# Optimization experiments

Hardware: AMD Instinct MI355X
Metric: run time of the kernel (lower is better)

## Reference

```python
import jax, jax.numpy as jnp
import numpy as np
from jax import lax

STRIDE = 1
PAD = 1  # module pads 1 on each side whenever padding != 0


def setup_inputs() -> dict:
    key = jax.random.key(0)
    kx, kw, kb = jax.random.split(key, 3)
    x = jax.random.normal(kx, (4096, 4096), dtype=jnp.float32)
    weight = jax.random.normal(kw, (15, 15), dtype=jnp.float32)
    bias = jax.random.normal(kb, (1,), dtype=jnp.float32)
    return {"x": x, "weight": weight, "bias": bias}


def reference(x, weight, bias):
    # Single-channel 2D cross-correlation with constant zero padding of 1 and
    # stride STRIDE, plus a scalar bias. lax.conv_general_dilated computes
    # correlation (no kernel flip), matching the torch corr2d loop exactly.
    out = lax.conv_general_dilated(
        x[None, None, :, :],          # NCHW, N=C=1
        weight[None, None, :, :],      # OIHW, O=I=1
        window_strides=(STRIDE, STRIDE),
        padding=[(PAD, PAD), (PAD, PAD)],
        dimension_numbers=("NCHW", "OIHW", "NCHW"),
    )[0, 0]
    return out + bias[0]
```

## Files before the change

### kernel.cpp

```cpp
#include <hip/hip_runtime.h>

#define IN_N   4096
#define OW     4084
#define KS     15
#define TILE   64
#define XROWS  78
#define XS     88
#define NBX    64
#define NBY    64

typedef __attribute__((ext_vector_type(8))) short     v8s;
typedef __attribute__((ext_vector_type(8))) _Float16  v8h;
typedef __attribute__((ext_vector_type(4))) float     v4f;
typedef __attribute__((ext_vector_type(2))) float     v2f;
typedef __attribute__((ext_vector_type(2))) unsigned  v2u;

__global__ void build_B(const float* __restrict__ w, unsigned short* __restrict__ Bg) {
    int ky = blockIdx.x;
    int e  = threadIdx.x;
    int n = e & 15, quad = e >> 4;
    unsigned short vals[8];
    #pragma unroll
    for (int j = 0; j < 8; ++j) {
        int d = quad * 8 + j - 1 - n;
        _Float16 h = (_Float16)0.0f;
        if (d >= 0 && d < KS) h = (_Float16)w[ky * KS + d];
        union { _Float16 hh; unsigned short u; } cv; cv.hh = h;
        vals[j] = cv.u;
    }
    *(v8s*)(&Bg[(ky * 64 + e) * 8]) = *(const v8s*)vals;
}

__device__ __forceinline__ unsigned pk(float a, float b) {
    return __builtin_bit_cast(unsigned, __builtin_amdgcn_cvt_pkrtz(a, b));
}

__global__ __launch_bounds__(256, 6) void conv2d_mfma10(
    const float* __restrict__ x, const unsigned short* __restrict__ Bg,
    const float* __restrict__ bias, float* __restrict__ out)
{
    __shared__ unsigned short xtile[XROWS * XS] __attribute__((aligned(16)));

    const int tid = threadIdx.x;
    const int bx = blockIdx.x, by = blockIdx.y;
    const int X0 = bx * TILE;
    const int Y0 = by * TILE;
    const bool interior = (bx > 0) & (bx < NBX - 1) & (by > 0) & (by < NBY - 1);

    if (tid < 240) {
        const int tcol = tid % 20;
        const int trow = tid / 20;
        const int c0 = 4 * tcol;
        unsigned short* dst = &xtile[trow * XS + c0];
        if (interior) {
            v2f Ld[7][2];
            const float* xr = x + (size_t)(Y0 - 1 + trow) * IN_N + (X0 - 2 + c0);
            #pragma unroll
            for (int i = 0; i < 7; ++i) {
                if (i < 6 || trow < 6) {
                    Ld[i][0] = *(const v2f*)xr;
                    Ld[i][1] = *(const v2f*)(xr + 2);
                }
                xr += 12 * (size_t)IN_N;
            }
            #pragma unroll
            for (int i = 0; i < 7; ++i) {
                if (i < 6 || trow < 6) {
                    v2u p;
                    p.x = pk(Ld[i][0].x, Ld[i][0].y);
                    p.y = pk(Ld[i][1].x, Ld[i][1].y);
                    *(v2u*)dst = p;
                }
                dst += 12 * XS;
            }
        } else {
            const int gc0 = X0 - 2 + c0;
            #pragma unroll
            for (int i = 0; i < 7; ++i) {
                int row = trow + 12 * i;
                if (row < XROWS) {
                    int gr = Y0 - 1 + row;
                    float f0 = 0.f, f1 = 0.f, f2 = 0.f, f3 = 0.f;
                    if ((unsigned)gr < (unsigned)IN_N) {
                        const float* xr = x + (size_t)gr * IN_N;
                        if ((unsigned)(gc0 + 0) < (unsigned)IN_N) f0 = xr[gc0 + 0];
                        if ((unsigned)(gc0 + 1) < (unsigned)IN_N) f1 = xr[gc0 + 1];
                        if ((unsigned)(gc0 + 2) < (unsigned)IN_N) f2 = xr[gc0 + 2];
                        if ((unsigned)(gc0 + 3) < (unsigned)IN_N) f3 = xr[gc0 + 3];
                    }
                    v2u p;
                    p.x = pk(f0, f1);
                    p.y = pk(f2, f3);
                    *(v2u*)(&xtile[row * XS + c0]) = p;
                }
            }
        }
    }
    __syncthreads();

    const int lane = tid & 63;
    const int wv   = tid >> 6;
    const int m    = lane & 15;
    const int quad = lane >> 4;

    v4f acc[4];
    #pragma unroll
    for (int t = 0; t < 4; ++t) acc[t] = (v4f){0.f, 0.f, 0.f, 0.f};

    const v8h* Bgv = (const v8h*)Bg;
    v8h bcur = Bgv[lane];
    const unsigned short* arow = &xtile[(wv * 16 + m) * XS + quad * 8];

    #pragma unroll
    for (int ky = 0; ky < KS; ++ky) {
        v8h bnext = (ky < KS - 1) ? Bgv[(ky + 1) * 64 + lane] : bcur;
        v8h a0 = *(const v8h*)(arow + 0);
        v8h a1 = *(const v8h*)(arow + 16);
        v8h a2 = *(const v8h*)(arow + 32);
        v8h a3 = *(const v8h*)(arow + 48);
        acc[0] = __builtin_amdgcn_mfma_f32_16x16x32_f16(a0, bcur, acc[0], 0, 0, 0);
        acc[1] = __builtin_amdgcn_mfma_f32_16x16x32_f16(a1, bcur, acc[1], 0, 0, 0);
        acc[2] = __builtin_amdgcn_mfma_f32_16x16x32_f16(a2, bcur, acc[2], 0, 0, 0);
        acc[3] = __builtin_amdgcn_mfma_f32_16x16x32_f16(a3, bcur, acc[3], 0, 0, 0);
        arow += XS;
        bcur = bnext;
    }

    const float bv = bias[0];
    const int orow0 = Y0 + wv * 16 + quad * 4;
    const int ocol0 = X0 + m;
    if (interior | ((bx < NBX - 1) & (by < NBY - 1))) {
        float* o0 = &out[(size_t)orow0 * OW + ocol0];
        #pragma unroll
        for (int t = 0; t < 4; ++t) {
            #pragma unroll
            for (int r = 0; r < 4; ++r)
                o0[(size_t)r * OW + t * 16] = acc[t][r] + bv;
        }
    } else {
        #pragma unroll
        for (int t = 0; t < 4; ++t) {
            int oc = ocol0 + t * 16;
            if (oc < OW) {
                #pragma unroll
                for (int r = 0; r < 4; ++r) {
                    int orow = orow0 + r;
                    if (orow < OW)
                        out[(size_t)orow * OW + oc] = acc[t][r] + bv;
                }
            }
        }
    }
}

extern "C" void kernel_launch(void* const* d_in, const int* in_sizes, int n_in,
                              void* d_out, int out_size, void* d_ws, size_t ws_size,
                              hipStream_t stream) {
    const float* x    = (const float*)d_in[0];
    const float* w    = (const float*)d_in[1];
    const float* bias = (const float*)d_in[2];
    float* out        = (float*)d_out;
    unsigned short* Bg = (unsigned short*)d_ws;

    build_B<<<dim3(KS), dim3(64), 0, stream>>>(w, Bg);
    dim3 grid(NBX, NBY);
    conv2d_mfma10<<<grid, dim3(256), 0, stream>>>(x, Bg, bias, out);
}
```

Baseline: 138.7 us.

## Warp-specialize blocks into staging and compute groups with double-buffered tiles

Each 512-thread block now covers four vertically stacked 64x64 output tiles. Two 256-thread groups alternate roles, one staging the next tile into a second LDS buffer while the other runs MFMA on the current one. The goal is to overlap global loads with matrix compute inside a block. The cost is fewer blocks (a quarter of the grid), half of the threads idle during each phase, a block-wide barrier per step, and doubled LDS per block.

```diff
diff --git a/kernel.cpp b/kernel.cpp
--- a/kernel.cpp
+++ b/kernel.cpp
@@ -6,8 +6,10 @@
 #define TILE   64
 #define XROWS  78
 #define XS     88
+#define TPB    4
 #define NBX    64
-#define NBY    64
+#define NBY    16
+#define NRT    64
 
 typedef __attribute__((ext_vector_type(8))) short     v8s;
 typedef __attribute__((ext_vector_type(8))) _Float16  v8h;
@@ -35,71 +37,60 @@
     return __builtin_bit_cast(unsigned, __builtin_amdgcn_cvt_pkrtz(a, b));
 }
 
-__global__ __launch_bounds__(256, 6) void conv2d_mfma10(
-    const float* __restrict__ x, const unsigned short* __restrict__ Bg,
-    const float* __restrict__ bias, float* __restrict__ out)
+__device__ __forceinline__ void stage_tile(
+    const float* __restrict__ x, unsigned short* __restrict__ buf,
+    int gtid, int R0, int X0, bool fast)
 {
-    __shared__ unsigned short xtile[XROWS * XS] __attribute__((aligned(16)));
-
-    const int tid = threadIdx.x;
-    const int bx = blockIdx.x, by = blockIdx.y;
-    const int X0 = bx * TILE;
-    const int Y0 = by * TILE;
-    const bool interior = (bx > 0) & (bx < NBX - 1) & (by > 0) & (by < NBY - 1);
-
-    if (tid < 240) {
-        const int tcol = tid % 20;
-        const int trow = tid / 20;
-        const int c0 = 4 * tcol;
-        unsigned short* dst = &xtile[trow * XS + c0];
-        if (interior) {
-            v2f Ld[7][2];
-            const float* xr = x + (size_t)(Y0 - 1 + trow) * IN_N + (X0 - 2 + c0);
-            #pragma unroll
-            for (int i = 0; i < 7; ++i) {
-                if (i < 6 || trow < 6) {
-                    Ld[i][0] = *(const v2f*)xr;
-                    Ld[i][1] = *(const v2f*)(xr + 2);
+    if (gtid >= 240) return;
+    const int tcol = gtid % 20;
+    const int trow = gtid / 20;
+    const int c0 = 4 * tcol;
+    unsigned short* dst = &buf[trow * XS + c0];
+    if (fast) {
+        const float* xr = x + (size_t)(R0 - 1 + trow) * IN_N + (X0 - 2 + c0);
+        #pragma unroll
+        for (int i = 0; i < 7; ++i) {
+            if (i < 6 || trow < 6) {
+                v2f f01 = *(const v2f*)xr;
+                v2f f23 = *(const v2f*)(xr + 2);
+                v2u p;
+                p.x = pk(f01.x, f01.y);
+                p.y = pk(f23.x, f23.y);
+                *(v2u*)dst = p;
+            }
+            xr  += 12 * (size_t)IN_N;
+            dst += 12 * XS;
+        }
+    } else {
+        const int gc0 = X0 - 2 + c0;
+        #pragma unroll
+        for (int i = 0; i < 7; ++i) {
+            int row = trow + 12 * i;
+            if (row < XROWS) {
+                int gr = R0 - 1 + row;
+                float f0 = 0.f, f1 = 0.f, f2 = 0.f, f3 = 0.f;
+                if ((unsigned)gr < (unsigned)IN_N) {
+                    const float* xr = x + (size_t)gr * IN_N;
+                    if ((unsigned)(gc0 + 0) < (unsigned)IN_N) f0 = xr[gc0 + 0];
+                    if ((unsigned)(gc0 + 1) < (unsigned)IN_N) f1 = xr[gc0 + 1];
+                    if ((unsigned)(gc0 + 2) < (unsigned)IN_N) f2 = xr[gc0 + 2];
+                    if ((unsigned)(gc0 + 3) < (unsigned)IN_N) f3 = xr[gc0 + 3];
                 }
-                xr += 12 * (size_t)IN_N;
-            }
-            #pragma unroll
-            for (int i = 0; i < 7; ++i) {
-                if (i < 6 || trow < 6) {
-                    v2u p;
-                    p.x = pk(Ld[i][0].x, Ld[i][0].y);
-                    p.y = pk(Ld[i][1].x, Ld[i][1].y);
-                    *(v2u*)dst = p;
-                }
-                dst += 12 * XS;
-            }
-        } else {
-            const int gc0 = X0 - 2 + c0;
-            #pragma unroll
-            for (int i = 0; i < 7; ++i) {
-                int row = trow + 12 * i;
-                if (row < XROWS) {
-                    int gr = Y0 - 1 + row;
-                    float f0 = 0.f, f1 = 0.f, f2 = 0.f, f3 = 0.f;
-                    if ((unsigned)gr < (unsigned)IN_N) {
-                        const float* xr = x + (size_t)gr * IN_N;
-                        if ((unsigned)(gc0 + 0) < (unsigned)IN_N) f0 = xr[gc0 + 0];
-                        if ((unsigned)(gc0 + 1) < (unsigned)IN_N) f1 = xr[gc0 + 1];
-                        if ((unsigned)(gc0 + 2) < (unsigned)IN_N) f2 = xr[gc0 + 2];
-                        if ((unsigned)(gc0 + 3) < (unsigned)IN_N) f3 = xr[gc0 + 3];
-                    }
-                    v2u p;
-                    p.x = pk(f0, f1);
-                    p.y = pk(f2, f3);
-                    *(v2u*)(&xtile[row * XS + c0]) = p;
-                }
+                v2u p;
+                p.x = pk(f0, f1);
+                p.y = pk(f2, f3);
+                *(v2u*)(&buf[row * XS + c0]) = p;
             }
         }
     }
-    __syncthreads();
+}
 
-    const int lane = tid & 63;
-    const int wv   = tid >> 6;
+__device__ __forceinline__ void compute_tile(
+    const unsigned short* __restrict__ buf, const v8h* __restrict__ Bgv,
+    float* __restrict__ out, float bv, int gtid, int R0, int X0, bool safe)
+{
+    const int lane = gtid & 63;
+    const int wv   = gtid >> 6;
     const int m    = lane & 15;
     const int quad = lane >> 4;
 
@@ -107,9 +98,8 @@
     #pragma unroll
     for (int t = 0; t < 4; ++t) acc[t] = (v4f){0.f, 0.f, 0.f, 0.f};
 
-    const v8h* Bgv = (const v8h*)Bg;
     v8h bcur = Bgv[lane];
-    const unsigned short* arow = &xtile[(wv * 16 + m) * XS + quad * 8];
+    const unsigned short* arow = &buf[(wv * 16 + m) * XS + quad * 8];
 
     #pragma unroll
     for (int ky = 0; ky < KS; ++ky) {
@@ -126,10 +116,9 @@
         bcur = bnext;
     }
 
-    const float bv = bias[0];
-    const int orow0 = Y0 + wv * 16 + quad * 4;
+    const int orow0 = R0 + wv * 16 + quad * 4;
     const int ocol0 = X0 + m;
-    if (interior | ((bx < NBX - 1) & (by < NBY - 1))) {
+    if (safe) {
         float* o0 = &out[(size_t)orow0 * OW + ocol0];
         #pragma unroll
         for (int t = 0; t < 4; ++t) {
@@ -153,6 +142,38 @@
     }
 }
 
+__global__ __launch_bounds__(512, 8) void conv2d_mfma11(
+    const float* __restrict__ x, const unsigned short* __restrict__ Bg,
+    const float* __restrict__ bias, float* __restrict__ out)
+{
+    __shared__ unsigned short xt[2][XROWS * XS] __attribute__((aligned(16)));
+
+    const int tid  = threadIdx.x;
+    const int gtid = tid & 255;
+    const int grp  = tid >> 8;
+    const int bx = blockIdx.x, by = blockIdx.y;
+    const int X0  = bx * TILE;
+    const int RT0 = by * TPB;
+    const bool colInt = (bx >= 1) & (bx <= NBX - 2);
+    const float bv = bias[0];
+    const v8h* Bgv = (const v8h*)Bg;
+
+    #pragma unroll 1
+    for (int p = 0; p <= TPB; ++p) {
+        if ((p < TPB) & ((p & 1) == grp)) {
+            const int RT = RT0 + p;
+            stage_tile(x, xt[p & 1], gtid, RT * TILE, X0,
+                       colInt & (RT >= 1) & (RT <= NRT - 2));
+        } else if ((p >= 1) & (((p - 1) & 1) == grp)) {
+            const int RT = RT0 + p - 1;
+            compute_tile(xt[(p - 1) & 1], Bgv, out, bv, gtid,
+                         RT * TILE, X0,
+                         (bx < NBX - 1) & (RT < NRT - 1));
+        }
+        __syncthreads();
+    }
+}
+
 extern "C" void kernel_launch(void* const* d_in, const int* in_sizes, int n_in,
                               void* d_out, int out_size, void* d_ws, size_t ws_size,
                               hipStream_t stream) {
@@ -164,5 +185,5 @@
 
     build_B<<<dim3(KS), dim3(64), 0, stream>>>(w, Bg);
     dim3 grid(NBX, NBY);
-    conv2d_mfma10<<<grid, dim3(256), 0, stream>>>(x, Bg, bias, out);
+    conv2d_mfma11<<<grid, dim3(512), 0, stream>>>(x, Bg, bias, out);
 }
```

New measurement: 158.4 us. +14.2%, slower.
